# Kernel tuning notes

Hardware: AMD Instinct MI355X
Metric: run time of the kernel (lower is better)

The kernel has to match this reference:

```python
import jax, jax.numpy as jnp
import numpy as np

N = 8192        # num nodes (bs in the original docstring)
D_IN = 512      # input feature dim
HEADS = 8
DPH = 512 // HEADS  # size_per_head = hidden_size // num_heads
EDGE_P = 0.01   # adjacency density


def setup_inputs() -> dict:
    key = jax.random.key(0)
    k1, k2, k3 = jax.random.split(key, 3)
    H = jax.random.normal(k1, (N, D_IN), dtype=jnp.float32)
    # dense 0/1 adjacency, as passed to the layer before tf.sparse.from_dense
    adj = (jax.random.uniform(k2, (N, N)) < EDGE_P).astype(jnp.float32)
    # Glorot-uniform per-head projection kernels, stacked: (HEADS, D_IN, DPH)
    limit = float(np.sqrt(6.0 / (D_IN + DPH)))
    W = jax.random.uniform(k3, (HEADS, D_IN, DPH), jnp.float32, -limit, limit)
    b = jnp.zeros((HEADS, DPH), jnp.float32)
    return {"H": H, "adj": adj, "W": W, "b": b}


def reference(H, adj, W, b):
    # Per-head dense projection: H_ = H @ W_h  -> (HEADS, N, DPH)
    H_ = jnp.einsum('nd,hde->hne', H, W)
    # NOTE: the original layer computes a sparse sigmoid/softmax attention
    # (f1 + f2^T over adj) but never uses it: head_output uses raw adj.
    # Aggregation: adj @ H_ per head, plus bias; activation = tf.identity.
    out = jnp.einsum('nm,hme->hne', adj, H_) + b[:, None, :]  # (HEADS, N, DPH)
    # Concat heads along feature axis (head 0 first) -> (N, HEADS*DPH)
    return jnp.transpose(out, (1, 0, 2)).reshape(H.shape[0], HEADS * DPH)
```

## Files before the change

kernel.cpp:

```cpp
#include <hip/hip_runtime.h>
#include <hip/hip_bf16.h>

typedef __attribute__((ext_vector_type(8))) short short8;
typedef __attribute__((ext_vector_type(4))) float floatx4;
typedef __attribute__((ext_vector_type(4))) uint uintx4;

#define GN 8192
#define GD 512
#define GEMM_BLOCKS 512

static __device__ __forceinline__ ushort bf16bits(float x) {
  __hip_bfloat16 h = __float2bfloat16(x);
  return *(ushort*)&h;
}
static __device__ __forceinline__ float bf16f(uint u16) {
  return __uint_as_float(u16 << 16);
}

typedef __attribute__((address_space(1))) const void g1_void;
typedef __attribute__((address_space(3))) void l3_void;
static __device__ __forceinline__ void gl_lds16(const void* g, void* l) {
  __builtin_amdgcn_global_load_lds((g1_void*)g, (l3_void*)l, 16, 0, 0);
}

__global__ void detect_kernel(const uint* __restrict__ H, const uint* __restrict__ W,
                              const uint* __restrict__ adj, const uint* __restrict__ b,
                              int* __restrict__ flags, float* __restrict__ bias) {
  __shared__ int cH, cW, cA, cB;
  const int t = threadIdx.x;
  if (t == 0) { cH = 0; cW = 0; cA = 0; cB = 0; }
  __syncthreads();
  { const uint e = (H[t] >> 7) & 0xFFu; if (e >= 100u && e <= 140u) atomicAdd(&cH, 1); }
  { const uint e = (W[t] >> 7) & 0xFFu; if (e >= 100u && e <= 140u) atomicAdd(&cW, 1); }
  for (int i = t; i < 4096; i += 256)
    if ((adj[i] & 0xFFFFu) == 0x3F80u) atomicAdd(&cA, 1);
  if (b[t] != 0u) atomicAdd(&cB, 1);
  __syncthreads();
  const int hb = cH > 128, wb = cW > 128, ab = cA > 0;
  if (t == 0) { flags[0] = hb; flags[1] = wb; flags[2] = ab; }
  if (cB == 0) {
    bias[t] = 0.0f; bias[t + 256] = 0.0f;
  } else if (wb) {
    const ushort* bs = (const ushort*)b;
    bias[t] = bf16f(bs[t]); bias[t + 256] = bf16f(bs[t + 256]);
  } else {
    const float* bf = (const float*)b;
    bias[t] = bf[t]; bias[t + 256] = bf[t + 256];
  }
}

#define BM 128
#define BN 64
#define BK 64
#define LDK 72

#define SMEM_BYTES (BM * LDK * 2 + BN * LDK * 2)

__global__ __launch_bounds__(256) void proj_kernel(
    const void* __restrict__ Hv, const void* __restrict__ Wv,
    ushort* __restrict__ HPt, const int* __restrict__ flags) {
  __shared__ __align__(16) unsigned char smem[SMEM_BYTES];
  ushort* sA = (ushort*)smem;
  ushort* sB = (ushort*)(smem + BM * LDK * 2);
  const int tid = threadIdx.x;
  const int hb = flags[0];
  const int wb = flags[1];
  const int bn = blockIdx.x & 7;
  const int bm = blockIdx.x >> 3;
  const int m0 = bm * BM;
  const int lane = tid & 63;
  const int w = tid >> 6;
  const int wr = w >> 1, wc = w & 1;
  const int l15 = lane & 15, q = lane >> 4;

  floatx4 acc[4][2];
#pragma unroll
  for (int i = 0; i < 4; i++)
#pragma unroll
    for (int j = 0; j < 2; j++) acc[i][j] = (floatx4)0.0f;

  for (int k0 = 0; k0 < GD; k0 += BK) {
    __syncthreads();
    if (hb) {
      const ushort* H16 = (const ushort*)Hv;
      const int r = tid >> 3;
      const int kc = (tid & 7) * 8;
#pragma unroll
      for (int p = 0; p < 4; p++) {
        const int row = r + p * 32;
        const uint4 v = *(const uint4*)(H16 + (size_t)(m0 + row) * GD + k0 + kc);
        *(uint4*)(sA + row * LDK + kc) = v;
      }
    } else {
      const float* H32 = (const float*)Hv;
      const int r0 = tid >> 4;
      const int kc = (tid & 15) * 4;
#pragma unroll
      for (int p = 0; p < 8; p++) {
        const int row = r0 + p * 16;
        const float4 v = *(const float4*)(H32 + (size_t)(m0 + row) * GD + k0 + kc);
        ushort4 o;
        o.x = bf16bits(v.x); o.y = bf16bits(v.y);
        o.z = bf16bits(v.z); o.w = bf16bits(v.w);
        *(ushort4*)(sA + row * LDK + kc) = o;
      }
    }
    if (wb) {
      const ushort* Wh = (const ushort*)Wv + (size_t)bn * (512 * 64);
      const int kk = tid >> 3;
      const int e0 = (tid & 7) * 8;
#pragma unroll
      for (int p = 0; p < 2; p++) {
        const int k = kk + p * 32;
        const uint4 v = *(const uint4*)(Wh + (size_t)(k0 + k) * 64 + e0);
        const ushort* pv = (const ushort*)&v;
#pragma unroll
        for (int j = 0; j < 8; j++) sB[(e0 + j) * LDK + k] = pv[j];
      }
    } else {
      const float* Wh = (const float*)Wv + (size_t)bn * (512 * 64);
      const int kk = tid >> 4;
      const int e0 = (tid & 15) * 4;
#pragma unroll
      for (int p = 0; p < 4; p++) {
        const int k = kk + p * 16;
        const float4 v = *(const float4*)(Wh + (size_t)(k0 + k) * 64 + e0);
        sB[(e0 + 0) * LDK + k] = bf16bits(v.x);
        sB[(e0 + 1) * LDK + k] = bf16bits(v.y);
        sB[(e0 + 2) * LDK + k] = bf16bits(v.z);
        sB[(e0 + 3) * LDK + k] = bf16bits(v.w);
      }
    }
    __syncthreads();
#pragma unroll
    for (int kq = 0; kq < 2; kq++) {
      short8 af[4], bfv[2];
#pragma unroll
      for (int mt = 0; mt < 4; mt++)
        af[mt] = *(const short8*)(sA + (wr * 64 + mt * 16 + l15) * LDK + kq * 32 + q * 8);
#pragma unroll
      for (int ct = 0; ct < 2; ct++)
        bfv[ct] = *(const short8*)(sB + (wc * 32 + ct * 16 + l15) * LDK + kq * 32 + q * 8);
#pragma unroll
      for (int mt = 0; mt < 4; mt++)
#pragma unroll
        for (int ct = 0; ct < 2; ct++)
          acc[mt][ct] = __builtin_amdgcn_mfma_f32_16x16x32_bf16(
              af[mt], bfv[ct], acc[mt][ct], 0, 0, 0);
    }
  }
#pragma unroll
  for (int mt = 0; mt < 4; mt++)
#pragma unroll
    for (int ct = 0; ct < 2; ct++) {
      const int col = bn * 64 + wc * 32 + ct * 16 + l15;
      const int rowb = m0 + wr * 64 + mt * 16 + q * 4;
      ushort4 o;
      o.x = bf16bits(acc[mt][ct][0]);
      o.y = bf16bits(acc[mt][ct][1]);
      o.z = bf16bits(acc[mt][ct][2]);
      o.w = bf16bits(acc[mt][ct][3]);
      *(ushort4*)(HPt + (size_t)col * GN + rowb) = o;
    }
}

#define ABM 64
#define ABK 64
#define AKCH 4096
#define ANT (AKCH / ABK)
#define ALDA 72

__global__ __launch_bounds__(512, 2) void agg_kernel(
    const void* __restrict__ adjv, const ushort* __restrict__ HPt,
    float* __restrict__ pbuf, const int* __restrict__ flags) {
  __shared__ __align__(16) ushort sA[ABM * ALDA];
  __shared__ __align__(16) ushort sB[2][GD * 64];
  const int ab = flags[2];
  const int bid = blockIdx.x;
  const int kch = bid & 1;
  const int m0 = (bid >> 1) * ABM;
  const size_t kb = (size_t)kch * AKCH;
  const int tid = threadIdx.x;
  const int lane = tid & 63, w = tid >> 6;
  const int l15 = lane & 15, q = lane >> 4;

  const int brow = lane >> 3;
  const int bkc = ((lane & 7) ^ brow) * 8;
  const int an = tid >> 3;
  const int akc = (tid & 7) * 8;

  const ushort* adj16 = (const ushort*)adjv;
  const float* adj32 = (const float*)adjv;

  floatx4 acc[4][4];
#pragma unroll
  for (int i = 0; i < 4; i++)
#pragma unroll
    for (int j = 0; j < 4; j++) acc[i][j] = (floatx4)0.0f;

  floatx4 a0, a1;
  uintx4 au;

#define STAGE_B(K0, BUF)                                                  \
  {                                                                       \
    _Pragma("unroll")                                                     \
    for (int p = 0; p < 8; p++) {                                         \
      const int e = p * 64 + w * 8 + brow;                                \
      gl_lds16(HPt + (size_t)e * GN + kb + (K0) + bkc,                    \
               &sB[BUF][(p * 64 + w * 8) * 64]);                          \
    }                                                                     \
  }

#define LOAD_A(K0)                                                        \
  {                                                                       \
    if (ab) {                                                             \
      au = __builtin_nontemporal_load(                                    \
          (const uintx4*)(adj16 + (size_t)(m0 + an) * GN + kb + (K0) + akc)); \
    } else {                                                              \
      const float* src = adj32 + (size_t)(m0 + an) * GN + kb + (K0) + akc;\
      a0 = __builtin_nontemporal_load((const floatx4*)src);               \
      a1 = __builtin_nontemporal_load((const floatx4*)(src + 4));         \
    }                                                                     \
  }

#define WRITE_A()                                                         \
  {                                                                       \
    if (ab) {                                                             \
      *(uintx4*)(sA + an * ALDA + akc) = au;                              \
    } else {                                                              \
      ushort4 o0, o1;                                                     \
      o0.x = bf16bits(a0.x); o0.y = bf16bits(a0.y);                       \
      o0.z = bf16bits(a0.z); o0.w = bf16bits(a0.w);                       \
      o1.x = bf16bits(a1.x); o1.y = bf16bits(a1.y);                       \
      o1.z = bf16bits(a1.z); o1.w = bf16bits(a1.w);                       \
      *(ushort4*)(sA + an * ALDA + akc) = o0;                             \
      *(ushort4*)(sA + an * ALDA + akc + 4) = o1;                        \
    }                                                                     \
  }

  STAGE_B(0, 0)
  LOAD_A(0)
  WRITE_A()
  __syncthreads();

  int cur = 0;
  for (int k = 0; k < ANT; ++k) {
    const int k1 = (k + 1) * ABK;
    if (k + 1 < ANT) {
      STAGE_B(k1, cur ^ 1)
      LOAD_A(k1)
    }
#pragma unroll
    for (int kq = 0; kq < 2; kq++) {
      short8 af[4], bfr[4];
#pragma unroll
      for (int mt = 0; mt < 4; mt++)
        af[mt] = *(const short8*)(sA + (mt * 16 + l15) * ALDA + kq * 32 + q * 8);
#pragma unroll
      for (int ct = 0; ct < 4; ct++) {
        const int r = w * 64 + ct * 16 + l15;
        const int slot = (kq * 4 + q) ^ (l15 & 7);
        bfr[ct] = *(const short8*)(&sB[cur][r * 64 + slot * 8]);
      }
#pragma unroll
      for (int mt = 0; mt < 4; mt++)
#pragma unroll
        for (int ct = 0; ct < 4; ct++)
          acc[mt][ct] = __builtin_amdgcn_mfma_f32_16x16x32_bf16(
              af[mt], bfr[ct], acc[mt][ct], 0, 0, 0);
    }
    __syncthreads();
    if (k + 1 < ANT) WRITE_A()
    __syncthreads();
    cur ^= 1;
  }

  float* pb = pbuf + (size_t)kch * ((size_t)GN * GD);
#pragma unroll
  for (int mt = 0; mt < 4; mt++)
#pragma unroll
    for (int ct = 0; ct < 4; ct++) {
      const int col = w * 64 + ct * 16 + l15;
      const int rowb = m0 + mt * 16 + q * 4;
#pragma unroll
      for (int r = 0; r < 4; r++)
        __builtin_nontemporal_store(
            acc[mt][ct][r], pb + (size_t)(rowb + r) * GD + col);
    }
#undef STAGE_B
#undef LOAD_A
#undef WRITE_A
}

__global__ __launch_bounds__(256) void combine_kernel(
    const float* __restrict__ pbuf, const float* __restrict__ bias,
    float* __restrict__ out) {
  const int i = blockIdx.x * 256 + threadIdx.x;
  const size_t stride = (size_t)GN * GD / 4;
  const floatx4 p0 = __builtin_nontemporal_load((const floatx4*)pbuf + i);
  const floatx4 p1 = __builtin_nontemporal_load((const floatx4*)pbuf + stride + i);
  const floatx4 bb = *((const floatx4*)bias + (i & 127));
  floatx4 o;
  o.x = p0.x + p1.x + bb.x;
  o.y = p0.y + p1.y + bb.y;
  o.z = p0.z + p1.z + bb.z;
  o.w = p0.w + p1.w + bb.w;
  __builtin_nontemporal_store(o, (floatx4*)out + i);
}

extern "C" void kernel_launch(void* const* d_in, const int* in_sizes, int n_in,
                              void* d_out, int out_size, void* d_ws, size_t ws_size,
                              hipStream_t stream) {
  const void *H = d_in[0], *adj = d_in[1], *W = d_in[2], *b = d_in[3];
  for (int i = 0; i < n_in; i++) {
    const int s = in_sizes[i];
    if (s == GN * GN) adj = d_in[i];
    else if (s == GN * GD) H = d_in[i];
    else if (s == 8 * 512 * 64) W = d_in[i];
    else if (s == 512) b = d_in[i];
  }
  float* out = (float*)d_out;

  char* ws = (char*)d_ws;
  ushort* HPt  = (ushort*)ws;
  float*  bias = (float*)(ws + (size_t)GN * GD * 2);
  int*    flags= (int*)(ws + (size_t)GN * GD * 2 + 4096);
  float*  pbuf = (float*)(ws + (size_t)16 * 1024 * 1024);

  detect_kernel<<<1, 256, 0, stream>>>((const uint*)H, (const uint*)W,
                                       (const uint*)adj, (const uint*)b,
                                       flags, bias);
  proj_kernel<<<GEMM_BLOCKS, 256, 0, stream>>>(H, W, HPt, flags);
  agg_kernel<<<256, 512, 0, stream>>>(adj, HPt, pbuf, flags);
  combine_kernel<<<4096, 256, 0, stream>>>(pbuf, bias, out);
}
```

Measured before the change: 501.0 us.

## Compress adjacency to bitmask alongside projection and aggregate from bitmask

Extra blocks appended to the projection launch ballot each adjacency row into 64-bit masks. The aggregation kernel then reads these compact masks and expands them into bf16 ones and zeros in shared memory, instead of streaming and converting the full dense adjacency inside the MFMA loop. The aggregation tile grows to 128 rows with a 4-way K split, and the combine step now sums four partial buffers. This assumes adjacency entries are exactly 0 or 1. It also adds a mask write pass and roughly doubles the partial-sum traffic.

```diff
diff --git a/kernel.cpp b/kernel.cpp
--- a/kernel.cpp
+++ b/kernel.cpp
@@ -56,13 +56,41 @@
 
 #define SMEM_BYTES (BM * LDK * 2 + BN * LDK * 2)
 
-__global__ __launch_bounds__(256) void proj_kernel(
+__global__ __launch_bounds__(256) void fused_pm_kernel(
     const void* __restrict__ Hv, const void* __restrict__ Wv,
-    ushort* __restrict__ HPt, const int* __restrict__ flags) {
+    const void* __restrict__ adjv, ushort* __restrict__ HPt,
+    unsigned long long* __restrict__ mask, const int* __restrict__ flags) {
   __shared__ __align__(16) unsigned char smem[SMEM_BYTES];
+  const int tid = threadIdx.x;
+
+  if (blockIdx.x >= GEMM_BLOCKS) {
+    const int n = blockIdx.x - GEMM_BLOCKS;
+    const int ab = flags[2];
+    const int w = tid >> 6, lane = tid & 63;
+    if (ab) {
+      const ushort* arow = (const ushort*)adjv + (size_t)n * GN;
+#pragma unroll
+      for (int c = 0; c < 32; c++) {
+        const int chunk = c * 4 + w;
+        const ushort v = arow[chunk * 64 + lane];
+        const unsigned long long m = __ballot(v != 0);
+        if (lane == 0) mask[(size_t)n * 128 + chunk] = m;
+      }
+    } else {
+      const float* arow = (const float*)adjv + (size_t)n * GN;
+#pragma unroll
+      for (int c = 0; c < 32; c++) {
+        const int chunk = c * 4 + w;
+        const float v = __builtin_nontemporal_load(arow + chunk * 64 + lane);
+        const unsigned long long m = __ballot(v != 0.0f);
+        if (lane == 0) mask[(size_t)n * 128 + chunk] = m;
+      }
+    }
+    return;
+  }
+
   ushort* sA = (ushort*)smem;
   ushort* sB = (ushort*)(smem + BM * LDK * 2);
-  const int tid = threadIdx.x;
   const int hb = flags[0];
   const int wb = flags[1];
   const int bn = blockIdx.x & 7;
@@ -164,21 +192,20 @@
     }
 }
 
-#define ABM 64
+#define ABM 128
 #define ABK 64
-#define AKCH 4096
+#define AKCH 2048
 #define ANT (AKCH / ABK)
 #define ALDA 72
 
-__global__ __launch_bounds__(512, 2) void agg_kernel(
-    const void* __restrict__ adjv, const ushort* __restrict__ HPt,
-    float* __restrict__ pbuf, const int* __restrict__ flags) {
+__global__ __launch_bounds__(512) void agg_kernel(
+    const unsigned long long* __restrict__ mask, const ushort* __restrict__ HPt,
+    float* __restrict__ pbuf) {
   __shared__ __align__(16) ushort sA[ABM * ALDA];
   __shared__ __align__(16) ushort sB[2][GD * 64];
-  const int ab = flags[2];
   const int bid = blockIdx.x;
-  const int kch = bid & 1;
-  const int m0 = (bid >> 1) * ABM;
+  const int kch = bid & 3;
+  const int m0 = (bid >> 2) * ABM;
   const size_t kb = (size_t)kch * AKCH;
   const int tid = threadIdx.x;
   const int lane = tid & 63, w = tid >> 6;
@@ -186,20 +213,16 @@
 
   const int brow = lane >> 3;
   const int bkc = ((lane & 7) ^ brow) * 8;
-  const int an = tid >> 3;
-  const int akc = (tid & 7) * 8;
-
-  const ushort* adj16 = (const ushort*)adjv;
-  const float* adj32 = (const float*)adjv;
-
-  floatx4 acc[4][4];
-#pragma unroll
-  for (int i = 0; i < 4; i++)
+  const int arow = tid >> 2;
+  const int asub = tid & 3;
+
+  floatx4 acc[8][4];
+#pragma unroll
+  for (int i = 0; i < 8; i++)
 #pragma unroll
     for (int j = 0; j < 4; j++) acc[i][j] = (floatx4)0.0f;
 
-  floatx4 a0, a1;
-  uintx4 au;
+  unsigned long long mw;
 
 #define STAGE_B(K0, BUF)                                                  \
   {                                                                       \
@@ -213,29 +236,21 @@
 
 #define LOAD_A(K0)                                                        \
   {                                                                       \
-    if (ab) {                                                             \
-      au = __builtin_nontemporal_load(                                    \
-          (const uintx4*)(adj16 + (size_t)(m0 + an) * GN + kb + (K0) + akc)); \
-    } else {                                                              \
-      const float* src = adj32 + (size_t)(m0 + an) * GN + kb + (K0) + akc;\
-      a0 = __builtin_nontemporal_load((const floatx4*)src);               \
-      a1 = __builtin_nontemporal_load((const floatx4*)(src + 4));         \
-    }                                                                     \
+    mw = __builtin_nontemporal_load(                                      \
+        mask + (size_t)(m0 + arow) * 128 + ((kb + (K0)) >> 6));           \
   }
 
 #define WRITE_A()                                                         \
   {                                                                       \
-    if (ab) {                                                             \
-      *(uintx4*)(sA + an * ALDA + akc) = au;                              \
-    } else {                                                              \
-      ushort4 o0, o1;                                                     \
-      o0.x = bf16bits(a0.x); o0.y = bf16bits(a0.y);                       \
-      o0.z = bf16bits(a0.z); o0.w = bf16bits(a0.w);                       \
-      o1.x = bf16bits(a1.x); o1.y = bf16bits(a1.y);                       \
-      o1.z = bf16bits(a1.z); o1.w = bf16bits(a1.w);                       \
-      *(ushort4*)(sA + an * ALDA + akc) = o0;                             \
-      *(ushort4*)(sA + an * ALDA + akc + 4) = o1;                        \
-    }                                                                     \
+    const uint bits = (uint)((mw >> (asub * 16)) & 0xFFFFull);            \
+    uint u[8];                                                            \
+    _Pragma("unroll")                                                     \
+    for (int jj = 0; jj < 8; jj++)                                        \
+      u[jj] = (((bits >> (2 * jj)) & 1u) ? 0x3F80u : 0u) |                \
+              (((bits >> (2 * jj + 1)) & 1u) ? 0x3F800000u : 0u);         \
+    uint* dst = (uint*)(sA + arow * ALDA + asub * 16);                    \
+    ((uintx4*)dst)[0] = *(uintx4*)&u[0];                                  \
+    ((uintx4*)dst)[1] = *(uintx4*)&u[4];                                  \
   }
 
   STAGE_B(0, 0)
@@ -252,9 +267,9 @@
     }
 #pragma unroll
     for (int kq = 0; kq < 2; kq++) {
-      short8 af[4], bfr[4];
-#pragma unroll
-      for (int mt = 0; mt < 4; mt++)
+      short8 af[8], bfr[4];
+#pragma unroll
+      for (int mt = 0; mt < 8; mt++)
         af[mt] = *(const short8*)(sA + (mt * 16 + l15) * ALDA + kq * 32 + q * 8);
 #pragma unroll
       for (int ct = 0; ct < 4; ct++) {
@@ -263,7 +278,7 @@
         bfr[ct] = *(const short8*)(&sB[cur][r * 64 + slot * 8]);
       }
 #pragma unroll
-      for (int mt = 0; mt < 4; mt++)
+      for (int mt = 0; mt < 8; mt++)
 #pragma unroll
         for (int ct = 0; ct < 4; ct++)
           acc[mt][ct] = __builtin_amdgcn_mfma_f32_16x16x32_bf16(
@@ -277,7 +292,7 @@
 
   float* pb = pbuf + (size_t)kch * ((size_t)GN * GD);
 #pragma unroll
-  for (int mt = 0; mt < 4; mt++)
+  for (int mt = 0; mt < 8; mt++)
 #pragma unroll
     for (int ct = 0; ct < 4; ct++) {
       const int col = w * 64 + ct * 16 + l15;
@@ -297,14 +312,16 @@
     float* __restrict__ out) {
   const int i = blockIdx.x * 256 + threadIdx.x;
   const size_t stride = (size_t)GN * GD / 4;
-  const floatx4 p0 = __builtin_nontemporal_load((const floatx4*)pbuf + i);
-  const floatx4 p1 = __builtin_nontemporal_load((const floatx4*)pbuf + stride + i);
+  floatx4 s = __builtin_nontemporal_load((const floatx4*)pbuf + i);
+#pragma unroll
+  for (int j = 1; j < 4; j++) {
+    const floatx4 a = __builtin_nontemporal_load(
+        (const floatx4*)pbuf + j * stride + i);
+    s.x += a.x; s.y += a.y; s.z += a.z; s.w += a.w;
+  }
   const floatx4 bb = *((const floatx4*)bias + (i & 127));
   floatx4 o;
-  o.x = p0.x + p1.x + bb.x;
-  o.y = p0.y + p1.y + bb.y;
-  o.z = p0.z + p1.z + bb.z;
-  o.w = p0.w + p1.w + bb.w;
+  o.x = s.x + bb.x; o.y = s.y + bb.y; o.z = s.z + bb.z; o.w = s.w + bb.w;
   __builtin_nontemporal_store(o, (floatx4*)out + i);
 }
 
@@ -325,12 +342,15 @@
   ushort* HPt  = (ushort*)ws;
   float*  bias = (float*)(ws + (size_t)GN * GD * 2);
   int*    flags= (int*)(ws + (size_t)GN * GD * 2 + 4096);
-  float*  pbuf = (float*)(ws + (size_t)16 * 1024 * 1024);
+  unsigned long long* mask =
+      (unsigned long long*)(ws + (size_t)12 * 1024 * 1024);
+  float*  pbuf = (float*)(ws + (size_t)32 * 1024 * 1024);
 
   detect_kernel<<<1, 256, 0, stream>>>((const uint*)H, (const uint*)W,
                                        (const uint*)adj, (const uint*)b,
                                        flags, bias);
-  proj_kernel<<<GEMM_BLOCKS, 256, 0, stream>>>(H, W, HPt, flags);
-  agg_kernel<<<256, 512, 0, stream>>>(adj, HPt, pbuf, flags);
+  fused_pm_kernel<<<GEMM_BLOCKS + GN, 256, 0, stream>>>(H, W, adj, HPt,
+                                                        mask, flags);
+  agg_kernel<<<256, 512, 0, stream>>>(mask, HPt, pbuf);
   combine_kernel<<<4096, 256, 0, stream>>>(pbuf, bias, out);
 }
```

Result: slower. 565.6 us (+12.9%).
